# Kernel optimization log

Hardware: AMD Instinct MI355X
Metric: run time of the kernel (lower is better)

Reference implementation:

```python
import jax, jax.numpy as jnp
import numpy as np

T, B, D_IN, D_H = 512, 256, 128, 128


def setup_inputs() -> dict:
    key = jax.random.key(0)
    ks = jax.random.split(key, 13)
    D = D_IN + D_H
    s = 1.0 / np.sqrt(D)  # torch nn.Linear default init bound
    inp = {"inputs": jax.random.normal(ks[0], (T, B, D_IN), jnp.float32)}
    for i, n in enumerate(["forget", "input", "update", "output"]):
        inp[f"W_{n}"] = jax.random.uniform(ks[1 + 3 * i], (2, D), jnp.float32, -s, s)
        inp[f"b_{n}"] = jax.random.uniform(ks[2 + 3 * i], (2,), jnp.float32, -s, s)
        inp[f"theta_{n}"] = jax.random.uniform(ks[3 + 3 * i], (2,), jnp.float32, 0.0, 2.0 * np.pi)
    return inp


def _qgate(comb, W, b, theta):
    # SamplerQNN analytic form (2 qubits):
    #   RY(x0)RY(th0) on wire0, RY(x1)RY(th1) on wire1, CNOT(0,1), measure <Z0>.
    #   Consecutive RYs compose; Z0 commutes with CNOT (wire0 is control),
    #   so QLayer output = <Z0> = cos(x0 + th0). Wire-1 params do not affect it.
    z0 = comb @ W[0] + b[0]  # first row of the 2-dim Linear projection: (B,)
    return jnp.cos(z0 + theta[0])


def reference(inputs, W_forget, b_forget, theta_forget, W_input, b_input, theta_input,
              W_update, b_update, theta_update, W_output, b_output, theta_output):
    Bsz = inputs.shape[1]
    h0 = jnp.zeros((Bsz, D_H), inputs.dtype)
    c0 = jnp.zeros((Bsz, D_H), inputs.dtype)

    def step(carry, x_t):
        hx, cx = carry
        comb = jnp.concatenate([x_t, hx], axis=1)  # (B, D_IN + D_H)
        # per-batch scalar gate activations, broadcast over hidden dim
        f = jax.nn.sigmoid(_qgate(comb, W_forget, b_forget, theta_forget))[:, None]
        i = jax.nn.sigmoid(_qgate(comb, W_input, b_input, theta_input))[:, None]
        g = jnp.tanh(_qgate(comb, W_update, b_update, theta_update))[:, None]
        o = jax.nn.sigmoid(_qgate(comb, W_output, b_output, theta_output))[:, None]
        cx = f * cx + i * g
        hx = o * jnp.tanh(cx)
        return (hx, cx), hx

    (hx, cx), outputs = jax.lax.scan(step, (h0, c0), inputs)
    return outputs, hx, cx
```

## Files before the change

### kernel.cpp

```cpp
#include <hip/hip_runtime.h>
#include <hip/hip_bf16.h>


constexpr int T = 512;
constexpr int Bsz = 256;
constexpr int R = T * Bsz;
constexpr float INV2PI = 0.15915494309189535f;

typedef float f4v __attribute__((ext_vector_type(4)));

__global__ __launch_bounds__(256) void xz_kernel(
    const float* __restrict__ x,
    const float* __restrict__ Wf, const float* __restrict__ bf, const float* __restrict__ tf,
    const float* __restrict__ Wi, const float* __restrict__ bi, const float* __restrict__ ti,
    const float* __restrict__ Wu, const float* __restrict__ bu, const float* __restrict__ tu,
    const float* __restrict__ Wo, const float* __restrict__ bo, const float* __restrict__ to_,
    float4* __restrict__ xz)
{
    const int wglobal = blockIdx.x * 4 + (threadIdx.x >> 6);
    const int lane = threadIdx.x & 63;
    const int hl = lane & 31;
    const int half = lane >> 5;

    const float4 wfv = ((const float4*)Wf)[hl];
    const float4 wiv = ((const float4*)Wi)[hl];
    const float4 wuv = ((const float4*)Wu)[hl];
    const float4 wov = ((const float4*)Wo)[hl];

    const float cf = bf[0] + tf[0];
    const float ci = bi[0] + ti[0];
    const float cu = bu[0] + tu[0];
    const float co = bo[0] + to_[0];

    for (int it = 0; it < 8; ++it) {
        const int row = (it * 8192 + wglobal) * 2 + half;
        const float4 xv = *(const float4*)(x + (size_t)row * 128 + hl * 4);

        float pf = xv.x * wfv.x + xv.y * wfv.y + xv.z * wfv.z + xv.w * wfv.w;
        float pi = xv.x * wiv.x + xv.y * wiv.y + xv.z * wiv.z + xv.w * wiv.w;
        float pu = xv.x * wuv.x + xv.y * wuv.y + xv.z * wuv.z + xv.w * wuv.w;
        float po = xv.x * wov.x + xv.y * wov.y + xv.z * wov.z + xv.w * wov.w;

#pragma unroll
        for (int off = 16; off; off >>= 1) {
            pf += __shfl_xor(pf, off, 64);
            pi += __shfl_xor(pi, off, 64);
            pu += __shfl_xor(pu, off, 64);
            po += __shfl_xor(po, off, 64);
        }
        if (hl == 0) {
            xz[row] = make_float4((pf + cf) * INV2PI, (pi + ci) * INV2PI,
                                  (pu + cu) * INV2PI, (po + co) * INV2PI);
        }
    }
}

__device__ __forceinline__ float tanh9(float c) {
    const float y  = c * c;
    const float y2 = y * y;
    const float lo  = fmaf(y, -0.321470f, 0.999168f);
    const float hi  = fmaf(y, 0.0016407f, -0.0199491f);
    const float mid = fmaf(y, hi, 0.101498f);
    return c * fmaf(y2, mid, lo);
}

template<int CTRL>
__device__ __forceinline__ float dppq(float x) {
    return __builtin_bit_cast(float,
        __builtin_amdgcn_mov_dpp(__builtin_bit_cast(int, x), CTRL, 0xF, 0xF, true));
}

__device__ __forceinline__ float wsum(const float* __restrict__ W, int lane) {
    float s = W[128 + lane] + W[192 + lane];
#pragma unroll
    for (int off = 32; off; off >>= 1) s += __shfl_xor(s, off, 64);
    return s;
}

constexpr int BPB = 8;
constexpr int SCAN_BLOCKS = Bsz / BPB;

__global__ __launch_bounds__(256, 1) void scan_kernel(
    const float4* __restrict__ xz,
    const float* __restrict__ Wf, const float* __restrict__ Wi,
    const float* __restrict__ Wu, const float* __restrict__ Wo,
    float* __restrict__ hscan, float* __restrict__ cfin)
{
    __shared__ float4 zb4[T * BPB];
    __shared__ float  hb[T * 32];
    const int tid = threadIdx.x;
    const int bb = blockIdx.x * BPB;

#pragma unroll
    for (int k = 0; k < T * BPB / 256; ++k) {
        const int j = k * 256 + tid;
        zb4[j] = xz[(j >> 3) * Bsz + bb + (j & 7)];
    }

    const int l = tid & 63;
    const float swf = wsum(Wf, l) * INV2PI;
    const float swi = wsum(Wi, l) * INV2PI;
    const float swu = wsum(Wu, l) * INV2PI;
    const float swo = wsum(Wo, l) * INV2PI;

    __syncthreads();

    if (tid < BPB * 4) {
        const int q = tid & 3;
        const int batch = bb + (tid >> 2);

        const float sw = (q == 0) ? swf : (q == 1) ? swi : (q == 2) ? swu : swo;

        const bool tq = (q == 2);
        const float K0 = tq ? 0.0f       : 0.5f;
        const float K1 = tq ? 0.999318f  : 0.249976f;
        const float K3 = tq ? -0.319476f : -0.0206916f;
        const float K5 = tq ? 0.08315f   : 0.00188244f;

        const float* zl = (const float*)zb4 + tid;
        float* hw = hb + tid;

        float c = 0.0f, tc = 0.0f, os = 0.0f;

#define HSTEP(Y, HT, S)                                            \
    {                                                              \
        const float u  = fmaf(tc, os, (Y));                        \
        const float v  = __builtin_amdgcn_cosf(u);                 \
        const float v2 = v * v;                                    \
        const float t1 = fmaf(v2, K5, K3);                         \
        const float p  = fmaf(v2, t1, K1);                         \
        const float gown = fmaf(v, p, K0);                         \
        const float f = dppq<0x00>(gown);                          \
        const float i = dppq<0x55>(gown);                          \
        const float g = dppq<0xAA>(gown);                          \
        const float o = dppq<0xFF>(gown);                          \
        c  = fmaf(f, c, i * g);                                    \
        tc = tanh9(c);                                             \
        os = o * sw;                                               \
        (HT)[(S) * 32] = o * tc;                                   \
    }

        float p0 = zl[0 * 32], p1 = zl[1 * 32], p2 = zl[2 * 32], p3 = zl[3 * 32];
        float p4 = zl[4 * 32], p5 = zl[5 * 32], p6 = zl[6 * 32], p7 = zl[7 * 32];

        for (int tb = 0; tb < T - 8; tb += 8) {
            const float* zn = zl + (size_t)(tb + 8) * 32;
            const float n0 = zn[0 * 32];
            const float n1 = zn[1 * 32];
            const float n2 = zn[2 * 32];
            const float n3 = zn[3 * 32];
            const float n4 = zn[4 * 32];
            const float n5 = zn[5 * 32];
            const float n6 = zn[6 * 32];
            const float n7 = zn[7 * 32];
            float* ht = hw + (size_t)tb * 32;
            HSTEP(p0, ht, 0); HSTEP(p1, ht, 1); HSTEP(p2, ht, 2); HSTEP(p3, ht, 3);
            HSTEP(p4, ht, 4); HSTEP(p5, ht, 5); HSTEP(p6, ht, 6); HSTEP(p7, ht, 7);
            p0 = n0; p1 = n1; p2 = n2; p3 = n3;
            p4 = n4; p5 = n5; p6 = n6; p7 = n7;
        }
        {
            float* ht = hw + (size_t)(T - 8) * 32;
            HSTEP(p0, ht, 0); HSTEP(p1, ht, 1); HSTEP(p2, ht, 2); HSTEP(p3, ht, 3);
            HSTEP(p4, ht, 4); HSTEP(p5, ht, 5); HSTEP(p6, ht, 6); HSTEP(p7, ht, 7);
        }
#undef HSTEP

        cfin[batch] = c;
    }

    __syncthreads();

    for (int j = tid; j < T * BPB; j += 256) {
        const int t = j >> 3, bg = j & 7;
        hscan[t * Bsz + bb + bg] = hb[t * 32 + bg * 4];
    }
}

__global__ __launch_bounds__(256) void bcast_kernel(
    const float* __restrict__ hscan, const float* __restrict__ cfin,
    float4* __restrict__ out)
{
    const unsigned i = blockIdx.x * 256u + threadIdx.x;
    const unsigned row = i >> 5;
    float v;
    if (row < (unsigned)R) {
        v = hscan[row];
    } else {
        const unsigned r2 = row - (unsigned)R;
        v = (r2 < (unsigned)Bsz) ? hscan[(T - 1) * Bsz + r2] : cfin[r2 - (unsigned)Bsz];
    }
    const f4v val = {v, v, v, v};
    __builtin_nontemporal_store(val, (f4v*)&out[i]);
}

extern "C" void kernel_launch(void* const* d_in, const int* in_sizes, int n_in,
                              void* d_out, int out_size, void* d_ws, size_t ws_size,
                              hipStream_t stream)
{
    const float* x  = (const float*)d_in[0];
    const float* Wf = (const float*)d_in[1];
    const float* bf = (const float*)d_in[2];
    const float* tf = (const float*)d_in[3];
    const float* Wi = (const float*)d_in[4];
    const float* bi = (const float*)d_in[5];
    const float* ti = (const float*)d_in[6];
    const float* Wu = (const float*)d_in[7];
    const float* bu = (const float*)d_in[8];
    const float* tu = (const float*)d_in[9];
    const float* Wo = (const float*)d_in[10];
    const float* bo = (const float*)d_in[11];
    const float* to_ = (const float*)d_in[12];

    float* ws    = (float*)d_ws;
    float4* xz   = (float4*)ws;
    float* hscan = ws + 4 * R;
    float* cfin  = ws + 5 * R;

    xz_kernel<<<2048, 256, 0, stream>>>(x, Wf, bf, tf, Wi, bi, ti, Wu, bu, tu, Wo, bo, to_, xz);
    scan_kernel<<<SCAN_BLOCKS, 256, 0, stream>>>(xz, Wf, Wi, Wu, Wo, hscan, cfin);

    const int total_f4 = (R + 2 * Bsz) * 32;
    bcast_kernel<<<total_f4 / 256, 256, 0, stream>>>(hscan, cfin, (float4*)d_out);
}
```

Baseline: 71.93 us.

## Pipeline xz projection, chunked scan, and output broadcast across chunked launches

Replaces the three-kernel sequence with six launches of one combined kernel. In each launch, 32 blocks run the recurrence over a 128-step time chunk, carrying h and c across launches through workspace state, while the remaining blocks compute the input projection for the next chunk and broadcast the previous chunk's hidden states to the output. The goal is to overlap the memory-bound projection and broadcast with the latency-bound serial scan. In exchange it adds more kernel launches and global-memory h/c handoffs, and the scan blocks now write h directly to global memory every step.

```diff
diff --git a/kernel.cpp b/kernel.cpp
--- a/kernel.cpp
+++ b/kernel.cpp
@@ -5,55 +5,13 @@
 constexpr int T = 512;
 constexpr int Bsz = 256;
 constexpr int R = T * Bsz;
+constexpr int CH = 128;
+constexpr int NCH = T / CH;
+constexpr int MEMB = 2016;
+constexpr int GRID = 32 + MEMB;
 constexpr float INV2PI = 0.15915494309189535f;
 
 typedef float f4v __attribute__((ext_vector_type(4)));
-
-__global__ __launch_bounds__(256) void xz_kernel(
-    const float* __restrict__ x,
-    const float* __restrict__ Wf, const float* __restrict__ bf, const float* __restrict__ tf,
-    const float* __restrict__ Wi, const float* __restrict__ bi, const float* __restrict__ ti,
-    const float* __restrict__ Wu, const float* __restrict__ bu, const float* __restrict__ tu,
-    const float* __restrict__ Wo, const float* __restrict__ bo, const float* __restrict__ to_,
-    float4* __restrict__ xz)
-{
-    const int wglobal = blockIdx.x * 4 + (threadIdx.x >> 6);
-    const int lane = threadIdx.x & 63;
-    const int hl = lane & 31;
-    const int half = lane >> 5;
-
-    const float4 wfv = ((const float4*)Wf)[hl];
-    const float4 wiv = ((const float4*)Wi)[hl];
-    const float4 wuv = ((const float4*)Wu)[hl];
-    const float4 wov = ((const float4*)Wo)[hl];
-
-    const float cf = bf[0] + tf[0];
-    const float ci = bi[0] + ti[0];
-    const float cu = bu[0] + tu[0];
-    const float co = bo[0] + to_[0];
-
-    for (int it = 0; it < 8; ++it) {
-        const int row = (it * 8192 + wglobal) * 2 + half;
-        const float4 xv = *(const float4*)(x + (size_t)row * 128 + hl * 4);
-
-        float pf = xv.x * wfv.x + xv.y * wfv.y + xv.z * wfv.z + xv.w * wfv.w;
-        float pi = xv.x * wiv.x + xv.y * wiv.y + xv.z * wiv.z + xv.w * wiv.w;
-        float pu = xv.x * wuv.x + xv.y * wuv.y + xv.z * wuv.z + xv.w * wuv.w;
-        float po = xv.x * wov.x + xv.y * wov.y + xv.z * wov.z + xv.w * wov.w;
-
-#pragma unroll
-        for (int off = 16; off; off >>= 1) {
-            pf += __shfl_xor(pf, off, 64);
-            pi += __shfl_xor(pi, off, 64);
-            pu += __shfl_xor(pu, off, 64);
-            po += __shfl_xor(po, off, 64);
-        }
-        if (hl == 0) {
-            xz[row] = make_float4((pf + cf) * INV2PI, (pi + ci) * INV2PI,
-                                  (pu + cu) * INV2PI, (po + co) * INV2PI);
-        }
-    }
-}
 
 __device__ __forceinline__ float tanh9(float c) {
     const float y  = c * c;
@@ -77,35 +35,40 @@
     return s;
 }
 
-constexpr int BPB = 8;
-constexpr int SCAN_BLOCKS = Bsz / BPB;
-
-__global__ __launch_bounds__(256, 1) void scan_kernel(
-    const float4* __restrict__ xz,
-    const float* __restrict__ Wf, const float* __restrict__ Wi,
-    const float* __restrict__ Wu, const float* __restrict__ Wo,
-    float* __restrict__ hscan, float* __restrict__ cfin)
+__global__ __launch_bounds__(256) void pipe_kernel(
+    const int k,
+    const float* __restrict__ x,
+    const float* __restrict__ Wf, const float* __restrict__ bf, const float* __restrict__ tf,
+    const float* __restrict__ Wi, const float* __restrict__ bi, const float* __restrict__ ti,
+    const float* __restrict__ Wu, const float* __restrict__ bu, const float* __restrict__ tu,
+    const float* __restrict__ Wo, const float* __restrict__ bo, const float* __restrict__ to_,
+    float4* __restrict__ xz, float* __restrict__ hscan,
+    float* __restrict__ hstate, float* __restrict__ cstate,
+    float4* __restrict__ out4)
 {
-    __shared__ float4 zb4[T * BPB];
-    __shared__ float  hb[T * 32];
     const int tid = threadIdx.x;
-    const int bb = blockIdx.x * BPB;
+
+    if (blockIdx.x < 32) {
+        if (k < 0 || k >= NCH) return;
+        __shared__ float4 zb4[CH * 8];
+        const int bb = blockIdx.x * 8;
+        const int cb = k * CH;
 
 #pragma unroll
-    for (int k = 0; k < T * BPB / 256; ++k) {
-        const int j = k * 256 + tid;
-        zb4[j] = xz[(j >> 3) * Bsz + bb + (j & 7)];
-    }
-
-    const int l = tid & 63;
-    const float swf = wsum(Wf, l) * INV2PI;
-    const float swi = wsum(Wi, l) * INV2PI;
-    const float swu = wsum(Wu, l) * INV2PI;
-    const float swo = wsum(Wo, l) * INV2PI;
-
-    __syncthreads();
-
-    if (tid < BPB * 4) {
+        for (int it = 0; it < CH * 8 / 256; ++it) {
+            const int j = it * 256 + tid;
+            zb4[j] = xz[(size_t)(cb + (j >> 3)) * Bsz + bb + (j & 7)];
+        }
+
+        const int l = tid & 63;
+        const float swf = wsum(Wf, l) * INV2PI;
+        const float swi = wsum(Wi, l) * INV2PI;
+        const float swu = wsum(Wu, l) * INV2PI;
+        const float swo = wsum(Wo, l) * INV2PI;
+
+        __syncthreads();
+        if (tid >= 32) return;
+
         const int q = tid & 3;
         const int batch = bb + (tid >> 2);
 
@@ -118,32 +81,34 @@
         const float K5 = tq ? 0.08315f   : 0.00188244f;
 
         const float* zl = (const float*)zb4 + tid;
-        float* hw = hb + tid;
-
-        float c = 0.0f, tc = 0.0f, os = 0.0f;
-
-#define HSTEP(Y, HT, S)                                            \
+        float* hp = hscan + (size_t)cb * Bsz + batch;
+
+        float h, c;
+        if (k == 0) { h = 0.0f; c = 0.0f; }
+        else        { h = hstate[batch]; c = cstate[batch]; }
+
+#define HSTEP(Y)                                                   \
     {                                                              \
-        const float u  = fmaf(tc, os, (Y));                        \
+        const float u  = fmaf(h, sw, (Y));                         \
         const float v  = __builtin_amdgcn_cosf(u);                 \
         const float v2 = v * v;                                    \
         const float t1 = fmaf(v2, K5, K3);                         \
         const float p  = fmaf(v2, t1, K1);                         \
         const float gown = fmaf(v, p, K0);                         \
-        const float f = dppq<0x00>(gown);                          \
-        const float i = dppq<0x55>(gown);                          \
-        const float g = dppq<0xAA>(gown);                          \
-        const float o = dppq<0xFF>(gown);                          \
-        c  = fmaf(f, c, i * g);                                    \
-        tc = tanh9(c);                                             \
-        os = o * sw;                                               \
-        (HT)[(S) * 32] = o * tc;                                   \
+        const float f  = dppq<0x00>(gown);                         \
+        const float i  = dppq<0x55>(gown);                         \
+        const float g_ = dppq<0xAA>(gown);                         \
+        const float o  = dppq<0xFF>(gown);                         \
+        c = fmaf(f, c, i * g_);                                    \
+        h = o * tanh9(c);                                          \
+        *hp = h;                                                   \
+        hp += Bsz;                                                 \
     }
 
         float p0 = zl[0 * 32], p1 = zl[1 * 32], p2 = zl[2 * 32], p3 = zl[3 * 32];
         float p4 = zl[4 * 32], p5 = zl[5 * 32], p6 = zl[6 * 32], p7 = zl[7 * 32];
 
-        for (int tb = 0; tb < T - 8; tb += 8) {
+        for (int tb = 0; tb < CH - 8; tb += 8) {
             const float* zn = zl + (size_t)(tb + 8) * 32;
             const float n0 = zn[0 * 32];
             const float n1 = zn[1 * 32];
@@ -153,45 +118,81 @@
             const float n5 = zn[5 * 32];
             const float n6 = zn[6 * 32];
             const float n7 = zn[7 * 32];
-            float* ht = hw + (size_t)tb * 32;
-            HSTEP(p0, ht, 0); HSTEP(p1, ht, 1); HSTEP(p2, ht, 2); HSTEP(p3, ht, 3);
-            HSTEP(p4, ht, 4); HSTEP(p5, ht, 5); HSTEP(p6, ht, 6); HSTEP(p7, ht, 7);
+            HSTEP(p0); HSTEP(p1); HSTEP(p2); HSTEP(p3);
+            HSTEP(p4); HSTEP(p5); HSTEP(p6); HSTEP(p7);
             p0 = n0; p1 = n1; p2 = n2; p3 = n3;
             p4 = n4; p5 = n5; p6 = n6; p7 = n7;
         }
-        {
-            float* ht = hw + (size_t)(T - 8) * 32;
-            HSTEP(p0, ht, 0); HSTEP(p1, ht, 1); HSTEP(p2, ht, 2); HSTEP(p3, ht, 3);
-            HSTEP(p4, ht, 4); HSTEP(p5, ht, 5); HSTEP(p6, ht, 6); HSTEP(p7, ht, 7);
-        }
+        HSTEP(p0); HSTEP(p1); HSTEP(p2); HSTEP(p3);
+        HSTEP(p4); HSTEP(p5); HSTEP(p6); HSTEP(p7);
 #undef HSTEP
 
-        cfin[batch] = c;
-    }
-
-    __syncthreads();
-
-    for (int j = tid; j < T * BPB; j += 256) {
-        const int t = j >> 3, bg = j & 7;
-        hscan[t * Bsz + bb + bg] = hb[t * 32 + bg * 4];
-    }
-}
-
-__global__ __launch_bounds__(256) void bcast_kernel(
-    const float* __restrict__ hscan, const float* __restrict__ cfin,
-    float4* __restrict__ out)
-{
-    const unsigned i = blockIdx.x * 256u + threadIdx.x;
-    const unsigned row = i >> 5;
-    float v;
-    if (row < (unsigned)R) {
-        v = hscan[row];
-    } else {
-        const unsigned r2 = row - (unsigned)R;
-        v = (r2 < (unsigned)Bsz) ? hscan[(T - 1) * Bsz + r2] : cfin[r2 - (unsigned)Bsz];
-    }
-    const f4v val = {v, v, v, v};
-    __builtin_nontemporal_store(val, (f4v*)&out[i]);
+        hstate[batch] = h;
+        cstate[batch] = c;
+        return;
+    }
+
+    const int mb   = blockIdx.x - 32;
+    const int wv   = tid >> 6;
+    const int lane = tid & 63;
+    const int hl   = lane & 31;
+    const int half = lane >> 5;
+
+    if (k + 1 < NCH) {
+        const float4 wfv = ((const float4*)Wf)[hl];
+        const float4 wiv = ((const float4*)Wi)[hl];
+        const float4 wuv = ((const float4*)Wu)[hl];
+        const float4 wov = ((const float4*)Wo)[hl];
+        const float cf = bf[0] + tf[0];
+        const float ci = bi[0] + ti[0];
+        const float cu = bu[0] + tu[0];
+        const float co = bo[0] + to_[0];
+
+        const int slab = (k + 1) * CH * Bsz;
+        for (int p = mb * 4 + wv; p < CH * Bsz / 2; p += MEMB * 4) {
+            const int row = slab + 2 * p + half;
+            const float4 xv = *(const float4*)(x + (size_t)row * 128 + hl * 4);
+
+            float pf = xv.x * wfv.x + xv.y * wfv.y + xv.z * wfv.z + xv.w * wfv.w;
+            float pi = xv.x * wiv.x + xv.y * wiv.y + xv.z * wiv.z + xv.w * wiv.w;
+            float pu = xv.x * wuv.x + xv.y * wuv.y + xv.z * wuv.z + xv.w * wuv.w;
+            float po = xv.x * wov.x + xv.y * wov.y + xv.z * wov.z + xv.w * wov.w;
+
+#pragma unroll
+            for (int off = 16; off; off >>= 1) {
+                pf += __shfl_xor(pf, off, 64);
+                pi += __shfl_xor(pi, off, 64);
+                pu += __shfl_xor(pu, off, 64);
+                po += __shfl_xor(po, off, 64);
+            }
+            if (hl == 0) {
+                xz[row] = make_float4((pf + cf) * INV2PI, (pi + ci) * INV2PI,
+                                      (pu + cu) * INV2PI, (po + co) * INV2PI);
+            }
+        }
+    }
+
+    if (k >= 1 && k <= NCH) {
+        const int slabr = (k - 1) * CH * Bsz;
+        for (int j = mb * 256 + tid; j < CH * Bsz * 32; j += MEMB * 256) {
+            const int row = slabr + (j >> 5);
+            const float v = hscan[row];
+            const f4v val = {v, v, v, v};
+            __builtin_nontemporal_store(val, (f4v*)&out4[(size_t)row * 32 + (j & 31)]);
+        }
+    }
+
+    if (k == NCH) {
+        for (int j = mb * 256 + tid; j < 2 * Bsz * 32; j += MEMB * 256) {
+            const int kind = j >> 13;
+            const int r    = (j >> 5) & 255;
+            const int col  = j & 31;
+            const float v = kind ? cstate[r] : hscan[(size_t)(T - 1) * Bsz + r];
+            const f4v val = {v, v, v, v};
+            __builtin_nontemporal_store(
+                val, (f4v*)&out4[((size_t)R + (size_t)kind * Bsz + r) * 32 + col]);
+        }
+    }
 }
 
 extern "C" void kernel_launch(void* const* d_in, const int* in_sizes, int n_in,
@@ -212,14 +213,15 @@
     const float* bo = (const float*)d_in[11];
     const float* to_ = (const float*)d_in[12];
 
-    float* ws    = (float*)d_ws;
-    float4* xz   = (float4*)ws;
-    float* hscan = ws + 4 * R;
-    float* cfin  = ws + 5 * R;
-
-    xz_kernel<<<2048, 256, 0, stream>>>(x, Wf, bf, tf, Wi, bi, ti, Wu, bu, tu, Wo, bo, to_, xz);
-    scan_kernel<<<SCAN_BLOCKS, 256, 0, stream>>>(xz, Wf, Wi, Wu, Wo, hscan, cfin);
-
-    const int total_f4 = (R + 2 * Bsz) * 32;
-    bcast_kernel<<<total_f4 / 256, 256, 0, stream>>>(hscan, cfin, (float4*)d_out);
-}
+    float* ws     = (float*)d_ws;
+    float4* xz    = (float4*)ws;
+    float* hscan  = ws + 4 * R;
+    float* hstate = ws + 5 * R;
+    float* cstate = ws + 5 * R + Bsz;
+
+    for (int k = -1; k <= NCH; ++k) {
+        pipe_kernel<<<GRID, 256, 0, stream>>>(
+            k, x, Wf, bf, tf, Wi, bi, ti, Wu, bu, tu, Wo, bo, to_,
+            xz, hscan, hstate, cstate, (float4*)d_out);
+    }
+}
```

After: 60.21 us (median of 2 runs). 1.19x faster.
